# Kernel optimization log

Hardware: AMD Instinct MI355X
Metric: run time of the kernel (lower is better)

The kernel has to match this reference:

```python
import jax, jax.numpy as jnp
import numpy as np

QUERY_DIM = 512
CAAN_DIM = 512
HID = 30

def setup_inputs() -> dict:
    key = jax.random.key(0)
    ks = jax.random.split(key, 9)
    def lin(kk, out_d, in_d):
        lim = 1.0 / np.sqrt(in_d)
        return jax.random.uniform(kk, (out_d, in_d), jnp.float32, -lim, lim)
    R = jax.random.normal(ks[0], (8, 2048, QUERY_DIM), jnp.float32)
    return {
        "R": R,
        "Wq": lin(ks[1], CAAN_DIM, QUERY_DIM), "bq": jnp.zeros((CAAN_DIM,), jnp.float32),
        "Wk": lin(ks[2], CAAN_DIM, QUERY_DIM), "bk": jnp.zeros((CAAN_DIM,), jnp.float32),
        "Wv": lin(ks[3], CAAN_DIM, QUERY_DIM), "bv": jnp.zeros((CAAN_DIM,), jnp.float32),
        "W1": lin(ks[4], HID, CAAN_DIM), "b1": jax.random.uniform(ks[5], (HID,), jnp.float32, -1/np.sqrt(CAAN_DIM), 1/np.sqrt(CAAN_DIM)),
        "W2": lin(ks[6], 1, HID), "b2": jax.random.uniform(ks[7], (1,), jnp.float32, -1/np.sqrt(HID), 1/np.sqrt(HID)),
    }

def reference(R, Wq, bq, Wk, bk, Wv, bv, W1, b1, W2, b2):
    # Projections: [b, n, d]
    Q = jnp.einsum('bnq,dq->bnd', R, Wq) + bq
    K = jnp.einsum('bnq,dq->bnd', R, Wk) + bk
    V = jnp.einsum('bnq,dq->bnd', R, Wv) + bv
    dk = K.shape[-1]
    # Full score matrix, naive exp-normalize (no max subtraction) as in original
    gamma = jnp.einsum('bnd,bmd->bnm', Q, K) / jnp.sqrt(jnp.float32(dk))
    e = jnp.exp(gamma)
    saat = e / jnp.sum(e, axis=2, keepdims=True)  # [b, n, n]
    a = jnp.einsum('bnm,bmd->bnd', saat, V)       # [b, n, d]
    # fc head: CAAN_dim -> 30 -> 1, squeeze last dim
    h = jnp.einsum('bnd,hd->bnh', a, W1) + b1
    winner_score = (jnp.einsum('bnh,oh->bno', h, W2) + b2)[..., 0]
    return winner_score
```

## Files before the change

kernel.cpp:

```cpp
#include <hip/hip_runtime.h>
#include <math.h>

#define BATCH 8
#define SEQ 2048
#define DIM 512
#define MTOT (BATCH*SEQ)
#define HID 30

typedef short bf16x8 __attribute__((ext_vector_type(8)));
typedef float f32x4 __attribute__((ext_vector_type(4)));

__device__ __forceinline__ unsigned short f2bf(float f) {
  unsigned int u = __float_as_uint(f);
  unsigned int r = (u + 0x7FFFu + ((u >> 16) & 1u)) >> 16;
  return (unsigned short)r;
}
__device__ __forceinline__ float bf2f(unsigned short u) {
  return __uint_as_float((unsigned int)u << 16);
}

__device__ __forceinline__ void gload_lds16(const void* g, void* l) {
  __builtin_amdgcn_global_load_lds((const __attribute__((address_space(1))) void*)g,
                                   (__attribute__((address_space(3))) void*)l, 16, 0, 0);
}

__device__ __forceinline__ void gemm256_core(const unsigned short* __restrict__ gA,
                                             const unsigned short* __restrict__ gB,
                                             char* smem, f32x4 (&acc)[8][4]) {
  const int t = threadIdx.x;
  const int lane = t & 63;
  const int w = t >> 6;
  const int wr = w >> 2, wc = w & 3;
  const int lr = lane & 15, kc = lane >> 4;
  const int ss = (t & 7) ^ ((t >> 3) & 7);
  const unsigned short* gsrc = (ss < 4 ? gA : gB) + (size_t)(t >> 3) * DIM + (ss & 3) * 8;
  const uint32_t dbase = (uint32_t)(t & 448) * 16;

  auto stage = [&](int slot, int kt) {
#pragma unroll
    for (int q = 0; q < 4; ++q)
      gload_lds16(gsrc + (size_t)(q * 64) * DIM + kt * 32,
                  smem + slot * 32768 + q * 8192 + dbase);
  };

  stage(0, 0); stage(1, 1);
  asm volatile("s_waitcnt vmcnt(4)" ::: "memory");
  __builtin_amdgcn_s_barrier();
  asm volatile("" ::: "memory");

#pragma unroll
  for (int kt = 0; kt < 16; ++kt) {
    const char* Ab = smem + (kt % 3) * 32768;
    const int fslot = (kt + 2) % 3;
    const int src = (kt + 2 < 16) ? (kt + 2) : 15;
    bf16x8 bfr[4], af[4], af2[4];
#pragma unroll
    for (int j = 0; j < 4; ++j) {
      int r = wc * 64 + j * 16 + lr;
      bfr[j] = *(const bf16x8*)(Ab + r * 128 + (((4 + kc) ^ (r & 7)) << 4));
    }
#pragma unroll
    for (int i = 0; i < 4; ++i) {
      int r = wr * 128 + i * 16 + lr;
      af[i] = *(const bf16x8*)(Ab + r * 128 + ((kc ^ (r & 7)) << 4));
    }
    __builtin_amdgcn_sched_barrier(0);
#pragma unroll
    for (int i = 0; i < 4; ++i) {
      int r = wr * 128 + (i + 4) * 16 + lr;
      af2[i] = *(const bf16x8*)(Ab + r * 128 + ((kc ^ (r & 7)) << 4));
    }
    __builtin_amdgcn_sched_barrier(0);
    stage(fslot, src);
    __builtin_amdgcn_sched_barrier(0);
    __builtin_amdgcn_s_setprio(1);
#pragma unroll
    for (int i = 0; i < 4; ++i)
#pragma unroll
      for (int j = 0; j < 4; ++j)
        acc[i][j] = __builtin_amdgcn_mfma_f32_16x16x32_bf16(af[i], bfr[j], acc[i][j], 0, 0, 0);
    __builtin_amdgcn_s_setprio(0);
    __builtin_amdgcn_sched_barrier(0);
    __builtin_amdgcn_s_setprio(1);
#pragma unroll
    for (int i = 0; i < 4; ++i)
#pragma unroll
      for (int j = 0; j < 4; ++j)
        acc[i + 4][j] = __builtin_amdgcn_mfma_f32_16x16x32_bf16(af2[i], bfr[j], acc[i + 4][j], 0, 0, 0);
    __builtin_amdgcn_s_setprio(0);
    __builtin_amdgcn_sched_barrier(0);
    asm volatile("s_waitcnt vmcnt(4)" ::: "memory");
    __builtin_amdgcn_s_barrier();
    asm volatile("" ::: "memory");
  }
}

__device__ __forceinline__ void gemm256x128_core(const unsigned short* __restrict__ gA,
                                                 const unsigned short* __restrict__ gB,
                                                 char* smem, f32x4 (&acc)[4][4]) {
  const int t = threadIdx.x;
  const int lane = t & 63;
  const int w = t >> 6;
  const int wr = w >> 1, wc = w & 1;
  const int lr = lane & 15, kc = lane >> 4;
  const int ss = (t & 7) ^ ((t >> 3) & 7);
  const size_t srcoff = (size_t)(t >> 3) * DIM + ss * 8;
  const uint32_t dbase = (uint32_t)(t & 448) * 16;

  auto stage = [&](int kt) {
    char* slot = smem + (kt & 1) * 49152;
#pragma unroll
    for (int q = 0; q < 4; ++q)
      gload_lds16(gA + srcoff + (size_t)(q * 64) * DIM + kt * 64, slot + q * 8192 + dbase);
#pragma unroll
    for (int q = 0; q < 2; ++q)
      gload_lds16(gB + srcoff + (size_t)(q * 64) * DIM + kt * 64, slot + 32768 + q * 8192 + dbase);
  };

  stage(0);
  asm volatile("s_waitcnt vmcnt(0)" ::: "memory");
  __builtin_amdgcn_s_barrier();
  asm volatile("" ::: "memory");

#pragma unroll
  for (int kt = 0; kt < 8; ++kt) {
    const char* Ab = smem + (kt & 1) * 49152;
    const char* Bb = Ab + 32768;
    if (kt < 7) stage(kt + 1);
    __builtin_amdgcn_sched_barrier(0);
#pragma unroll
    for (int s = 0; s < 2; ++s) {
      bf16x8 bfr[4], af[4];
      const int ch = s * 4 + kc;
#pragma unroll
      for (int j = 0; j < 4; ++j) {
        int r = wc * 64 + j * 16 + lr;
        bfr[j] = *(const bf16x8*)(Bb + r * 128 + ((ch ^ (r & 7)) << 4));
      }
#pragma unroll
      for (int i = 0; i < 4; ++i) {
        int r = wr * 64 + i * 16 + lr;
        af[i] = *(const bf16x8*)(Ab + r * 128 + ((ch ^ (r & 7)) << 4));
      }
      __builtin_amdgcn_sched_barrier(0);
      __builtin_amdgcn_s_setprio(1);
#pragma unroll
      for (int i = 0; i < 4; ++i)
#pragma unroll
        for (int j = 0; j < 4; ++j)
          acc[i][j] = __builtin_amdgcn_mfma_f32_16x16x32_bf16(af[i], bfr[j], acc[i][j], 0, 0, 0);
      __builtin_amdgcn_s_setprio(0);
      __builtin_amdgcn_sched_barrier(0);
    }
    asm volatile("s_waitcnt vmcnt(0)" ::: "memory");
    __builtin_amdgcn_s_barrier();
    asm volatile("" ::: "memory");
  }
}

__global__ __launch_bounds__(256) void k_prep(
    const float* __restrict__ R, const float* __restrict__ Wq, const float* __restrict__ Wk,
    const float* __restrict__ Wv, const float* __restrict__ bq, const float* __restrict__ bv,
    const float* __restrict__ W1, const float* __restrict__ b1,
    const float* __restrict__ W2, const float* __restrict__ b2,
    unsigned short* __restrict__ Gt, unsigned short* __restrict__ Rb16,
    float* __restrict__ u, float* __restrict__ wv2, float* __restrict__ consts) {
  __shared__ __align__(16) float As[16][34];
  __shared__ __align__(16) float Bs[16][34];
  __shared__ float vecs[512];
  __shared__ float red2[16][17];
  const int bid = blockIdx.x;
  const int t = threadIdx.x;

  if (bid >= 321) {
    size_t base = ((size_t)(bid - 321) * 256 + t) * 8;
    float4 r0 = *(const float4*)&R[base];
    float4 r1 = *(const float4*)&R[base + 4];
    ushort4 lo, hi;
    lo.x = f2bf(r0.x); lo.y = f2bf(r0.y); lo.z = f2bf(r0.z); lo.w = f2bf(r0.w);
    hi.x = f2bf(r1.x); hi.y = f2bf(r1.y); hi.z = f2bf(r1.z); hi.w = f2bf(r1.w);
    *(ushort4*)&Rb16[base] = lo;
    *(ushort4*)&Rb16[base + 4] = hi;
    return;
  }
  if (bid < 256) {
    int tm = t & 15, tn = t >> 4;
    int q1b = (bid & 15) * 32, q2b = (bid >> 4) * 32;
    int lk = t >> 4, lc = (t & 15) * 2;
    float acc[2][2] = {};
    for (int kb = 0; kb < DIM; kb += 16) {
      *(float2*)&As[lk][lc] = *(const float2*)&Wq[(size_t)(kb + lk) * DIM + q1b + lc];
      *(float2*)&Bs[lk][lc] = *(const float2*)&Wk[(size_t)(kb + lk) * DIM + q2b + lc];
      __syncthreads();
#pragma unroll
      for (int k = 0; k < 16; ++k) {
        float a0 = As[k][tm * 2], a1 = As[k][tm * 2 + 1];
        float b0 = Bs[k][tn * 2], b1v = Bs[k][tn * 2 + 1];
        acc[0][0] = fmaf(a0, b0, acc[0][0]); acc[0][1] = fmaf(a0, b1v, acc[0][1]);
        acc[1][0] = fmaf(a1, b0, acc[1][0]); acc[1][1] = fmaf(a1, b1v, acc[1][1]);
      }
      __syncthreads();
    }
#pragma unroll
    for (int i = 0; i < 2; ++i)
#pragma unroll
      for (int j = 0; j < 2; ++j)
        Gt[(size_t)(q2b + tn * 2 + j) * DIM + (q1b + tm * 2 + i)] = f2bf(acc[i][j]);
    return;
  }
  if (bid < 320) {
    bool isU = bid < 288;
    int qb = (bid - (isU ? 256 : 288)) * 16;
    if (isU) {
      vecs[t] = bq[t];
      vecs[t + 256] = bq[t + 256];
    } else {
      for (int d = t; d < DIM; d += 256) {
        float s = 0.f;
        for (int j = 0; j < HID; ++j) s = fmaf(W2[j], W1[(size_t)j * DIM + d], s);
        vecs[d] = s;
      }
    }
    __syncthreads();
    const float* M = isU ? Wk : Wv;
    int ql = t & 15, ds = t >> 4;
    float s = 0.f;
#pragma unroll 8
    for (int i = 0; i < 32; ++i) {
      int d = ds * 32 + i;
      s = fmaf(vecs[d], M[(size_t)d * DIM + qb + ql], s);
    }
    red2[ds][ql] = s;
    __syncthreads();
    if (t < 16) {
      float r = 0.f;
#pragma unroll
      for (int k = 0; k < 16; ++k) r += red2[k][t];
      (isU ? u : wv2)[qb + t] = r;
    }
    return;
  }
  {
    for (int d = t; d < DIM; d += 256) {
      float s = 0.f;
      for (int j = 0; j < HID; ++j) s = fmaf(W2[j], W1[(size_t)j * DIM + d], s);
      vecs[d] = s;
    }
    __syncthreads();
    float* red = (float*)red2;
    red[t] = bv[t] * vecs[t] + bv[t + 256] * vecs[t + 256];
    __syncthreads();
    for (int o = 128; o > 0; o >>= 1) {
      if (t < o) red[t] += red[t + o];
      __syncthreads();
    }
    if (t == 0) {
      consts[0] = red[0];
      float s = b2[0];
      for (int j = 0; j < HID; ++j) s = fmaf(W2[j], b1[j], s);
      consts[1] = s;
    }
  }
}

__global__ __launch_bounds__(512, 2) void k_projT(const unsigned short* __restrict__ Rb16,
                                                  const unsigned short* __restrict__ Gt,
                                                  const float* __restrict__ u,
                                                  const float* __restrict__ wv2,
                                                  unsigned short* __restrict__ Tb16,
                                                  float* __restrict__ vw) {
  __shared__ __align__(16) char smem[98304];
  __shared__ float u_lds[128];
  int t = threadIdx.x;
  size_t rowb = (size_t)blockIdx.x * 256;
  int colb = blockIdx.y * 128;
  if (t < 128) u_lds[t] = u[colb + t];
  f32x4 acc[4][4] = {};
  gemm256x128_core(Rb16 + rowb * DIM, Gt + (size_t)colb * DIM, smem, acc);
  int lane = t & 63, w = t >> 6, wr = w >> 1, wc = w & 1;
  int lr = lane & 15, kq = lane >> 4;
#pragma unroll
  for (int i = 0; i < 4; ++i)
#pragma unroll
    for (int j = 0; j < 4; ++j)
#pragma unroll
      for (int r = 0; r < 4; ++r) {
        int row = wr * 64 + i * 16 + kq * 4 + r;
        int col = wc * 64 + j * 16 + lr;
        Tb16[(rowb + row) * DIM + colb + col] = f2bf(acc[i][j][r] + u_lds[col]);
      }
  if (blockIdx.y == 0) {
    float* wv2s = (float*)smem;
    __syncthreads();
    if (t < 512) { wv2s[t] = wv2[t]; }
    __syncthreads();
    int row = (int)rowb + (t >> 1);
    const unsigned short* rp = Rb16 + (size_t)row * DIM + (t & 1) * 256;
    const float* wp = wv2s + (t & 1) * 256;
    float s = 0.f;
#pragma unroll 8
    for (int i = 0; i < 32; ++i) {
      bf16x8 v = *(const bf16x8*)(rp + i * 8);
#pragma unroll
      for (int e = 0; e < 8; ++e) s = fmaf(bf2f((unsigned short)v[e]), wp[i * 8 + e], s);
    }
    s += __shfl_xor(s, 1);
    if ((t & 1) == 0) vw[row] = s;
  }
}

__global__ __launch_bounds__(512, 2) void k_qk(const unsigned short* __restrict__ Tb16,
                                               const unsigned short* __restrict__ Rb16,
                                               const float* __restrict__ vw,
                                               float* __restrict__ part_s1,
                                               float* __restrict__ part_den) {
  __shared__ __align__(16) char smem[98304];
  __shared__ float vw_lds[256];
  __shared__ float red_s1[4][256], red_den[4][256];
  int t = threadIdx.x;
  int orig = blockIdx.x;
  int wgid = (orig & 7) * 64 + (orig >> 3);
  int b = wgid >> 6;
  int nb = ((wgid >> 3) & 7) * 256;
  int mb = (wgid & 7) * 256;
  if (t < 256) vw_lds[t] = vw[b * SEQ + mb + t];
  f32x4 acc[8][4] = {};
  gemm256_core(Tb16 + ((size_t)b * SEQ + nb) * DIM,
               Rb16 + ((size_t)b * SEQ + mb) * DIM, smem, acc);
  int lane = t & 63, w = t >> 6, wr = w >> 2, wc = w & 3;
  int lr = lane & 15, kq = lane >> 4;
  const float rs = 0.044194173824159216f;
  float vwl[4];
#pragma unroll
  for (int j = 0; j < 4; ++j) vwl[j] = vw_lds[wc * 64 + j * 16 + lr];
#pragma unroll
  for (int i = 0; i < 8; ++i) {
#pragma unroll
    for (int r = 0; r < 4; ++r) {
      float sa = 0.f, sd = 0.f;
#pragma unroll
      for (int j = 0; j < 4; ++j) {
        float e = __expf(acc[i][j][r] * rs);
        sa = fmaf(e, vwl[j], sa);
        sd += e;
      }
#pragma unroll
      for (int m = 1; m < 16; m <<= 1) { sa += __shfl_xor(sa, m); sd += __shfl_xor(sd, m); }
      if (lr == 0) {
        int rl = wr * 128 + i * 16 + kq * 4 + r;
        red_s1[wc][rl] = sa;
        red_den[wc][rl] = sd;
      }
    }
  }
  __syncthreads();
  if (t < 256) {
    size_t o = ((size_t)b * 8 + (mb >> 8)) * SEQ + nb + t;
    part_s1[o] = red_s1[0][t] + red_s1[1][t] + red_s1[2][t] + red_s1[3][t];
    part_den[o] = red_den[0][t] + red_den[1][t] + red_den[2][t] + red_den[3][t];
  }
}

__global__ void k_final(const float* __restrict__ part_s1, const float* __restrict__ part_den,
                        const float* __restrict__ consts, float* __restrict__ out) {
  int n = blockIdx.x * 256 + threadIdx.x;
  int b = n >> 11, nn = n & 2047;
  float s1 = 0.f, dn = 0.f;
#pragma unroll
  for (int i = 0; i < 8; ++i) {
    size_t o = ((size_t)b * 8 + i) * SEQ + nn;
    s1 += part_s1[o];
    dn += part_den[o];
  }
  out[n] = s1 / dn + consts[0] + consts[1];
}

extern "C" void kernel_launch(void* const* d_in, const int* in_sizes, int n_in,
                              void* d_out, int out_size, void* d_ws, size_t ws_size,
                              hipStream_t stream) {
  const float* R  = (const float*)d_in[0];
  const float* Wq = (const float*)d_in[1];
  const float* bq = (const float*)d_in[2];
  const float* Wk = (const float*)d_in[3];
  const float* bk = (const float*)d_in[4];
  const float* Wv = (const float*)d_in[5];
  const float* bv = (const float*)d_in[6];
  const float* W1 = (const float*)d_in[7];
  const float* b1 = (const float*)d_in[8];
  const float* W2 = (const float*)d_in[9];
  const float* b2 = (const float*)d_in[10];
  (void)bk;
  float* out = (float*)d_out;

  char* p = (char*)d_ws;
  unsigned short* Rb16 = (unsigned short*)p; p += (size_t)MTOT * DIM * 2;
  unsigned short* Tb16 = (unsigned short*)p; p += (size_t)MTOT * DIM * 2;
  unsigned short* Gt   = (unsigned short*)p; p += (size_t)DIM * DIM * 2;
  float* part_s1  = (float*)p; p += (size_t)BATCH * 8 * SEQ * 4;
  float* part_den = (float*)p; p += (size_t)BATCH * 8 * SEQ * 4;
  float* u      = (float*)p; p += DIM * 4;
  float* wv2    = (float*)p; p += DIM * 4;
  float* vw     = (float*)p; p += MTOT * 4;
  float* consts = (float*)p; p += 16;

  hipLaunchKernelGGL(k_prep, dim3(321 + MTOT * DIM / (256 * 8)), dim3(256), 0, stream,
                     R, Wq, Wk, Wv, bq, bv, W1, b1, W2, b2, Gt, Rb16, u, wv2, consts);
  hipLaunchKernelGGL(k_projT, dim3(MTOT / 256, DIM / 128), dim3(512), 0, stream,
                     Rb16, Gt, u, wv2, Tb16, vw);
  hipLaunchKernelGGL(k_qk, dim3(512), dim3(512), 0, stream, Tb16, Rb16, vw, part_s1, part_den);
  hipLaunchKernelGGL(k_final, dim3(MTOT / 256), dim3(256), 0, stream,
                     part_s1, part_den, consts, out);
}
```

Before: 98.21 us.

## Use 256x256 tiles in projection GEMM and prefetch weights in prep

The projection kernel k_projT now reuses the existing 256x256 GEMM core (the one k_qk already uses) in place of the 256x128 core, which halves the column-block grid and doubles the per-block output tile. This cuts how often Rb16 tiles are reloaded and raises data reuse, at the cost of more accumulator registers per thread and fewer blocks in flight. The prep kernel's Wq/Wk tile loop also register-prefetches the next k-slice while the current one is computed. The unused 256x128 core is removed, and an explicit vmcnt wait is added before LDS is reused for wv2.

```diff
diff --git a/kernel.cpp b/kernel.cpp
--- a/kernel.cpp
+++ b/kernel.cpp
@@ -90,69 +90,6 @@
     __builtin_amdgcn_s_setprio(0);
     __builtin_amdgcn_sched_barrier(0);
     asm volatile("s_waitcnt vmcnt(4)" ::: "memory");
-    __builtin_amdgcn_s_barrier();
-    asm volatile("" ::: "memory");
-  }
-}
-
-__device__ __forceinline__ void gemm256x128_core(const unsigned short* __restrict__ gA,
-                                                 const unsigned short* __restrict__ gB,
-                                                 char* smem, f32x4 (&acc)[4][4]) {
-  const int t = threadIdx.x;
-  const int lane = t & 63;
-  const int w = t >> 6;
-  const int wr = w >> 1, wc = w & 1;
-  const int lr = lane & 15, kc = lane >> 4;
-  const int ss = (t & 7) ^ ((t >> 3) & 7);
-  const size_t srcoff = (size_t)(t >> 3) * DIM + ss * 8;
-  const uint32_t dbase = (uint32_t)(t & 448) * 16;
-
-  auto stage = [&](int kt) {
-    char* slot = smem + (kt & 1) * 49152;
-#pragma unroll
-    for (int q = 0; q < 4; ++q)
-      gload_lds16(gA + srcoff + (size_t)(q * 64) * DIM + kt * 64, slot + q * 8192 + dbase);
-#pragma unroll
-    for (int q = 0; q < 2; ++q)
-      gload_lds16(gB + srcoff + (size_t)(q * 64) * DIM + kt * 64, slot + 32768 + q * 8192 + dbase);
-  };
-
-  stage(0);
-  asm volatile("s_waitcnt vmcnt(0)" ::: "memory");
-  __builtin_amdgcn_s_barrier();
-  asm volatile("" ::: "memory");
-
-#pragma unroll
-  for (int kt = 0; kt < 8; ++kt) {
-    const char* Ab = smem + (kt & 1) * 49152;
-    const char* Bb = Ab + 32768;
-    if (kt < 7) stage(kt + 1);
-    __builtin_amdgcn_sched_barrier(0);
-#pragma unroll
-    for (int s = 0; s < 2; ++s) {
-      bf16x8 bfr[4], af[4];
-      const int ch = s * 4 + kc;
-#pragma unroll
-      for (int j = 0; j < 4; ++j) {
-        int r = wc * 64 + j * 16 + lr;
-        bfr[j] = *(const bf16x8*)(Bb + r * 128 + ((ch ^ (r & 7)) << 4));
-      }
-#pragma unroll
-      for (int i = 0; i < 4; ++i) {
-        int r = wr * 64 + i * 16 + lr;
-        af[i] = *(const bf16x8*)(Ab + r * 128 + ((ch ^ (r & 7)) << 4));
-      }
-      __builtin_amdgcn_sched_barrier(0);
-      __builtin_amdgcn_s_setprio(1);
-#pragma unroll
-      for (int i = 0; i < 4; ++i)
-#pragma unroll
-        for (int j = 0; j < 4; ++j)
-          acc[i][j] = __builtin_amdgcn_mfma_f32_16x16x32_bf16(af[i], bfr[j], acc[i][j], 0, 0, 0);
-      __builtin_amdgcn_s_setprio(0);
-      __builtin_amdgcn_sched_barrier(0);
-    }
-    asm volatile("s_waitcnt vmcnt(0)" ::: "memory");
     __builtin_amdgcn_s_barrier();
     asm volatile("" ::: "memory");
   }
@@ -188,10 +125,16 @@
     int q1b = (bid & 15) * 32, q2b = (bid >> 4) * 32;
     int lk = t >> 4, lc = (t & 15) * 2;
     float acc[2][2] = {};
+    float2 ra = *(const float2*)&Wq[(size_t)lk * DIM + q1b + lc];
+    float2 rb = *(const float2*)&Wk[(size_t)lk * DIM + q2b + lc];
     for (int kb = 0; kb < DIM; kb += 16) {
-      *(float2*)&As[lk][lc] = *(const float2*)&Wq[(size_t)(kb + lk) * DIM + q1b + lc];
-      *(float2*)&Bs[lk][lc] = *(const float2*)&Wk[(size_t)(kb + lk) * DIM + q2b + lc];
+      *(float2*)&As[lk][lc] = ra;
+      *(float2*)&Bs[lk][lc] = rb;
       __syncthreads();
+      if (kb + 16 < DIM) {
+        ra = *(const float2*)&Wq[(size_t)(kb + 16 + lk) * DIM + q1b + lc];
+        rb = *(const float2*)&Wk[(size_t)(kb + 16 + lk) * DIM + q2b + lc];
+      }
 #pragma unroll
       for (int k = 0; k < 16; ++k) {
         float a0 = As[k][tm * 2], a1 = As[k][tm * 2 + 1];
@@ -270,29 +213,30 @@
                                                   unsigned short* __restrict__ Tb16,
                                                   float* __restrict__ vw) {
   __shared__ __align__(16) char smem[98304];
-  __shared__ float u_lds[128];
+  __shared__ float u_lds[256];
   int t = threadIdx.x;
   size_t rowb = (size_t)blockIdx.x * 256;
-  int colb = blockIdx.y * 128;
-  if (t < 128) u_lds[t] = u[colb + t];
-  f32x4 acc[4][4] = {};
-  gemm256x128_core(Rb16 + rowb * DIM, Gt + (size_t)colb * DIM, smem, acc);
-  int lane = t & 63, w = t >> 6, wr = w >> 1, wc = w & 1;
+  int colb = blockIdx.y * 256;
+  if (t < 256) u_lds[t] = u[colb + t];
+  f32x4 acc[8][4] = {};
+  gemm256_core(Rb16 + rowb * DIM, Gt + (size_t)colb * DIM, smem, acc);
+  int lane = t & 63, w = t >> 6, wr = w >> 2, wc = w & 3;
   int lr = lane & 15, kq = lane >> 4;
 #pragma unroll
-  for (int i = 0; i < 4; ++i)
+  for (int i = 0; i < 8; ++i)
 #pragma unroll
     for (int j = 0; j < 4; ++j)
 #pragma unroll
       for (int r = 0; r < 4; ++r) {
-        int row = wr * 64 + i * 16 + kq * 4 + r;
+        int row = wr * 128 + i * 16 + kq * 4 + r;
         int col = wc * 64 + j * 16 + lr;
         Tb16[(rowb + row) * DIM + colb + col] = f2bf(acc[i][j][r] + u_lds[col]);
       }
   if (blockIdx.y == 0) {
+    asm volatile("s_waitcnt vmcnt(0)" ::: "memory");
+    __syncthreads();
     float* wv2s = (float*)smem;
-    __syncthreads();
-    if (t < 512) { wv2s[t] = wv2[t]; }
+    wv2s[t] = wv2[t];
     __syncthreads();
     int row = (int)rowb + (t >> 1);
     const unsigned short* rp = Rb16 + (size_t)row * DIM + (t & 1) * 256;
@@ -405,7 +349,7 @@
 
   hipLaunchKernelGGL(k_prep, dim3(321 + MTOT * DIM / (256 * 8)), dim3(256), 0, stream,
                      R, Wq, Wk, Wv, bq, bv, W1, b1, W2, b2, Gt, Rb16, u, wv2, consts);
-  hipLaunchKernelGGL(k_projT, dim3(MTOT / 256, DIM / 128), dim3(512), 0, stream,
+  hipLaunchKernelGGL(k_projT, dim3(MTOT / 256, DIM / 256), dim3(512), 0, stream,
                      Rb16, Gt, u, wv2, Tb16, vw);
   hipLaunchKernelGGL(k_qk, dim3(512), dim3(512), 0, stream, Tb16, Rb16, vw, part_s1, part_den);
   hipLaunchKernelGGL(k_final, dim3(MTOT / 256), dim3(256), 0, stream,
```

After: 93.07 us. -5.2%, faster.
